# Kernel optimization log

Hardware: AMD Instinct MI355X
Metric: run time of the kernel (lower is better)

## Reference

```python
import jax, jax.numpy as jnp
import numpy as np

B, T, N, H = 1024, 256, 32, 64  # batch, SEQ_LEN, N_SERIES, RNN_HID_SIZE
EPS = 1e-05


def setup_inputs() -> dict:
    key = jax.random.key(0)
    ks = jax.random.split(key, 24)
    s_h = 1.0 / np.sqrt(H)
    s_n = 1.0 / np.sqrt(N)
    u = lambda k, shape, s: jax.random.uniform(k, shape, jnp.float32, -s, s)
    inp = {
        'values': jax.random.normal(ks[0], (B, T, N), jnp.float32),
        'masks': (jax.random.uniform(ks[1], (B, T, N)) < 0.8).astype(jnp.float32),
        'deltas': jax.random.uniform(ks[2], (B, T, N), jnp.float32) * 5.0,
        'evals': jax.random.normal(ks[3], (B, T, N), jnp.float32),
        'eval_masks': (jax.random.uniform(ks[4], (B, T, N)) < 0.1).astype(jnp.float32),
        'labels': (jax.random.uniform(ks[5], (B, 1)) < 0.5).astype(jnp.float32),
        'is_train': jnp.ones((B, 1), jnp.float32),
        # TemporalDecay h: Linear(N->H)
        'td_h_W': u(ks[6], (H, N), s_h), 'td_h_b': u(ks[7], (H,), s_h),
        # TemporalDecay x: diag Linear(N->N)
        'td_x_W': u(ks[8], (N, N), s_n), 'td_x_b': u(ks[9], (N,), s_n),
        # hist_reg: Linear(H->N)
        'hist_W': u(ks[10], (N, H), s_n), 'hist_b': u(ks[11], (N,), s_n),
        # feat_reg: masked Linear(N->N), mask = 1 - I
        'feat_W': u(ks[12], (N, N), s_n), 'feat_b': u(ks[13], (N,), s_n),
        # weight_combine: Linear(2N->N)
        'wc_W': u(ks[14], (N, 2 * N), s_n), 'wc_b': u(ks[15], (N,), s_n),
        # LSTMCell(2N -> H)
        'W_ih': u(ks[16], (4 * H, 2 * N), s_h), 'W_hh': u(ks[17], (4 * H, H), s_h),
        'b_ih': u(ks[18], (4 * H,), s_h), 'b_hh': u(ks[19], (4 * H,), s_h),
        # out: Linear(H->1)
        'out_W': u(ks[20], (1, H), s_h), 'out_b': u(ks[21], (1,), s_h),
    }
    return inp


def _rits_forward(values, masks, deltas, labels, is_train,
                  td_h_W, td_h_b, td_x_W, td_x_b, hist_W, hist_b,
                  feat_W, feat_b, wc_W, wc_b, W_ih, W_hh, b_ih, b_hh,
                  out_W, out_b):
    # time-major for scan: [T, B, N]
    vals_t = jnp.swapaxes(values, 0, 1)
    masks_t = jnp.swapaxes(masks, 0, 1)
    delts_t = jnp.swapaxes(deltas, 0, 1)

    feat_mask = 1.0 - jnp.eye(N, dtype=values.dtype)
    td_x_diag = jnp.diagonal(td_x_W)                  # W * eye(N) linear == elementwise diag

    def step(carry, xmd):
        h, c, x_loss = carry
        x, m, d = xmd
        gamma_h = jnp.exp(-jax.nn.relu(d @ td_h_W.T + td_h_b))   # [B,H]
        gamma_x = jnp.exp(-jax.nn.relu(d * td_x_diag + td_x_b))  # [B,N]
        h = h * gamma_h
        x_h = h @ hist_W.T + hist_b
        msum = jnp.sum(m) + EPS
        x_loss = x_loss + jnp.sum(jnp.abs(x - x_h) * m) / msum
        x_c = m * x + (1.0 - m) * x_h
        z_h = x_c @ (feat_W * feat_mask).T + feat_b
        x_loss = x_loss + jnp.sum(jnp.abs(x - z_h) * m) / msum
        alpha = jnp.concatenate([gamma_x, m], axis=1) @ wc_W.T + wc_b
        c_h = alpha * z_h + (1.0 - alpha) * x_h
        x_loss = x_loss + jnp.sum(jnp.abs(x - c_h) * m) / msum
        c_c = m * x + (1.0 - m) * c_h
        inputs = jnp.concatenate([c_c, m], axis=1)  # [B, 2N]
        gates = inputs @ W_ih.T + b_ih + h @ W_hh.T + b_hh
        i, f, g, o = jnp.split(gates, 4, axis=1)
        c = jax.nn.sigmoid(f) * c + jax.nn.sigmoid(i) * jnp.tanh(g)
        h = jax.nn.sigmoid(o) * jnp.tanh(c)
        return (h, c, x_loss), c_c

    h0 = jnp.zeros((values.shape[0], H), values.dtype)
    c0 = jnp.zeros((values.shape[0], H), values.dtype)
    (h, c, x_loss), imps = jax.lax.scan(step, (h0, c0, jnp.float32(0.0)),
                                        (vals_t, masks_t, delts_t))
    imputations = jnp.swapaxes(imps, 0, 1)  # [B, T, N]

    y_h = h @ out_W.T + out_b  # logits [B,1]
    # binary_cross_entropy_with_logits, reduce=False
    max_val = jnp.maximum(-y_h, 0.0)
    bce = y_h - y_h * labels + max_val + jnp.log(jnp.exp(-max_val) + jnp.exp(-y_h - max_val))
    y_loss = jnp.sum(bce * is_train) / (jnp.sum(is_train) + EPS)
    loss = x_loss / T + y_loss * 0.1
    predictions = jax.nn.sigmoid(y_h)
    return loss, predictions, imputations


def reference(values, masks, deltas, evals, eval_masks, labels, is_train,
              td_h_W, td_h_b, td_x_W, td_x_b, hist_W, hist_b, feat_W, feat_b,
              wc_W, wc_b, W_ih, W_hh, b_ih, b_hh, out_W, out_b):
    loss, predictions, imputations = _rits_forward(
        values, masks, deltas, labels, is_train,
        td_h_W, td_h_b, td_x_W, td_x_b, hist_W, hist_b,
        feat_W, feat_b, wc_W, wc_b, W_ih, W_hh, b_ih, b_hh, out_W, out_b)
    return loss, predictions, imputations
```

## Files before the change

### kernel.cpp

```cpp
#include <hip/hip_runtime.h>

#define EPSF 1e-5f

typedef _Float16 h2f  __attribute__((ext_vector_type(2)));
typedef _Float16 h8   __attribute__((ext_vector_type(8)));
typedef float    f32x4 __attribute__((ext_vector_type(4)));

#if defined(__has_builtin)
#if __has_builtin(__builtin_amdgcn_fdot2)
#define HAVE_FDOT2 1
#endif
#endif

__device__ __forceinline__ float fsig(float x){ return 1.0f/(1.0f+__expf(-x)); }
__device__ __forceinline__ float ftanh(float x){
  float e = __expf(2.f*x);
  float r = (e-1.f)/(e+1.f);
  return (x > 15.f) ? 1.f : ((x < -15.f) ? -1.f : r);
}
__device__ __forceinline__ int pkf(float lo, float hi){
  return __builtin_bit_cast(int, __builtin_amdgcn_cvt_pkrtz(lo, hi));
}
__device__ __forceinline__ int4 mk4(const float* p){
  return make_int4(pkf(p[0],p[1]),pkf(p[2],p[3]),pkf(p[4],p[5]),pkf(p[6],p[7]));
}
__device__ __forceinline__ float dot2(int w, int x, float acc){
#ifdef HAVE_FDOT2
  return __builtin_amdgcn_fdot2(__builtin_bit_cast(h2f, w),
                                __builtin_bit_cast(h2f, x), acc, false);
#else
  h2f a = __builtin_bit_cast(h2f, w), b = __builtin_bit_cast(h2f, x);
  return acc + (float)a[0]*(float)b[0] + (float)a[1]*(float)b[1];
#endif
}
__device__ __forceinline__ int rl_i(int v, int l){ return __builtin_amdgcn_readlane(v, l); }
__device__ __forceinline__ float rl_f(float v, int l){
  return __int_as_float(__builtin_amdgcn_readlane(__float_as_int(v), l));
}
#define MFMA(A,B,C) __builtin_amdgcn_mfma_f32_16x16x32_f16( \
    __builtin_bit_cast(h8,(A)), __builtin_bit_cast(h8,(B)), (C), 0,0,0)
#define BAR() do{ asm volatile("s_waitcnt lgkmcnt(0)" ::: "memory"); __builtin_amdgcn_s_barrier(); }while(0)

__global__ void msum_kernel(const float* __restrict__ masks, float* __restrict__ msum){
  const int t   = blockIdx.x;
  const int tid = threadIdx.x;
  const int b0  = tid >> 3;
  const int n4  = (tid & 7) << 2;
  float s = 0.f;
  #pragma unroll 4
  for (int i = 0; i < 32; ++i) {
    const int b = b0 + (i << 5);
    const float4 v = *reinterpret_cast<const float4*>(masks + ((size_t)b*256 + t)*32 + n4);
    s += v.x + v.y + v.z + v.w;
  }
  __shared__ float red[256];
  red[tid] = s; __syncthreads();
  for (int off = 128; off > 0; off >>= 1) {
    if (tid < off) red[tid] += red[tid + off];
    __syncthreads();
  }
  if (tid == 0) msum[t] = red[0] + EPSF;
}

__global__ __launch_bounds__(512)
__attribute__((amdgpu_waves_per_eu(2, 2)))
void rits_kernel(
  const float* __restrict__ values, const float* __restrict__ masks,
  const float* __restrict__ deltas, const float* __restrict__ labels,
  const float* __restrict__ is_train,
  const float* __restrict__ td_h_W, const float* __restrict__ td_h_b,
  const float* __restrict__ td_x_W, const float* __restrict__ td_x_b,
  const float* __restrict__ hist_W, const float* __restrict__ hist_b,
  const float* __restrict__ feat_W, const float* __restrict__ feat_b,
  const float* __restrict__ wc_W,  const float* __restrict__ wc_b,
  const float* __restrict__ W_ih,  const float* __restrict__ W_hh,
  const float* __restrict__ b_ih,  const float* __restrict__ b_hh,
  const float* __restrict__ out_W, const float* __restrict__ out_b,
  const float* __restrict__ msum,
  float* __restrict__ xl_acc, float* __restrict__ bce_acc,
  float* __restrict__ predictions, float* __restrict__ imps)
{
  __shared__ __align__(16) int  inp_s[4][84];
  __shared__ __align__(16) int  nb[4][52];
  __shared__ float sB[4][64];
  __shared__ float sAl[4][32];
  __shared__ float gp[4][256];
  __shared__ float msum_l[256];

  const int tid = threadIdx.x;
  const int b   = blockIdx.x;
  const int wv  = tid >> 6;
  const int ln  = tid & 63;
  const bool chain = (wv < 4);
  const int me  = wv & 3;
  const int b2  = (b << 2) | me;
  const int kg  = ln >> 4;
  const int arow = ln & 15;

  if (tid < 256) msum_l[tid] = 1.0f / msum[tid];

  int4 Wb[2][4];
  #pragma unroll
  for (int nt = 0; nt < 2; ++nt){
    const int col = (wv << 5) + (nt << 4) + (ln & 15);
    #pragma unroll
    for (int ks = 0; ks < 4; ++ks){
      const int k0 = (ks << 5) + (kg << 3);
      const float* src = (k0 < 64) ? (W_ih + (size_t)col*64 + k0)
                                   : (W_hh + (size_t)col*64 + (k0 - 64));
      Wb[nt][ks] = make_int4(pkf(src[0],src[1]), pkf(src[2],src[3]),
                             pkf(src[4],src[5]), pkf(src[6],src[7]));
    }
  }
  const int col0 = (wv << 5) + (ln & 15);
  const float bs0 = b_ih[col0]      + b_hh[col0];
  const float bs1 = b_ih[col0 + 16] + b_hh[col0 + 16];

  int4 fGh = make_int4(0,0,0,0);
  float ghb = 0.f; int colj = 0;
  int4 fA0 = make_int4(0,0,0,0), fA1 = make_int4(0,0,0,0);
  float alb = 0.f; int colA = 0;
  if (wv >= 4){
    colj = ((wv - 4) << 4) | (ln & 15);
    fGh  = mk4(td_h_W + colj*32 + kg*8);
    ghb  = td_h_b[colj];
    if (wv < 6){
      colA = ((wv - 4) << 4) | (ln & 15);
      fA0  = mk4(wc_W + colA*64 + kg*8);
      fA1  = mk4(wc_W + colA*64 + 32 + kg*8);
      alb  = wc_b[colA];
    }
  }

  int4  fC[8];
  float wz[32];
  float tdxd_r=0.f, tdxb_r=0.f, histb_r=0.f, featb_r=0.f;
  float xv=0.f, mv=0.f, dv=0.f;
  if (chain){
    const int nr = ln & 31;
    #pragma unroll
    for (int g = 0; g < 8; ++g) fC[g] = mk4(hist_W + nr*64 + 8*g);
    #pragma unroll
    for (int k = 0; k < 32; ++k) wz[k] = (k==nr) ? 0.f : feat_W[nr*32 + k];
    if (ln < 32){
      tdxd_r  = td_x_W[ln*33];
      tdxb_r  = td_x_b[ln];
      histb_r = hist_b[ln];
      featb_r = feat_b[ln];
      const size_t base = (size_t)b2*8192 + ln;
      xv = values[base]; mv = masks[base]; dv = deltas[base];
    }
  }
  float h_reg = 0.f, c_reg = 0.f, loss_acc = 0.f;
  const int i0 = (2*ln) & 63, i1 = (2*ln+1) & 63;

  __syncthreads();

  if (chain && ln < 32){
    _Float16* np = reinterpret_cast<_Float16*>(&nb[me][0]);
    const float gx0 = __expf(-fmaxf(fmaf(dv, tdxd_r, tdxb_r), 0.f));
    np[ln]      = (_Float16)dv;
    np[32 + ln] = (_Float16)gx0;
    np[64 + ln] = (_Float16)mv;
  }
  __syncthreads();
  if (wv >= 4){
    int4 A = make_int4(0,0,0,0);
    if (arow < 4) A = *reinterpret_cast<const int4*>(&nb[arow][kg << 2]);
    f32x4 acc = {ghb, ghb, ghb, ghb};
    acc = MFMA(A, fGh, acc);
    if (kg == 0){
      #pragma unroll
      for (int e = 0; e < 4; ++e) sB[e][colj] = acc[e];
    }
    if (wv < 6){
      int4 A0 = make_int4(0,0,0,0), A1 = make_int4(0,0,0,0);
      if (arow < 4){
        A0 = *reinterpret_cast<const int4*>(&nb[arow][16 + (kg << 2)]);
        A1 = *reinterpret_cast<const int4*>(&nb[arow][32 + (kg << 2)]);
      }
      f32x4 aacc = {alb, alb, alb, alb};
      aacc = MFMA(A0, fA0, aacc);
      aacc = MFMA(A1, fA1, aacc);
      if (kg == 0){
        #pragma unroll
        for (int e = 0; e < 4; ++e) sAl[e][colA] = aacc[e];
      }
    }
  }
  __syncthreads();

  for (int t = 0; t < 256; ++t){
    if (chain){
      const float x_cur = xv, m_cur = mv;
      const float sb = sB[me][ln];
      const float al = (ln < 32) ? sAl[me][ln] : 0.f;
      if (ln < 32 && t < 255){
        const size_t base = (size_t)b2*8192 + (size_t)(t+1)*32 + ln;
        xv = values[base]; mv = masks[base]; dv = deltas[base];
      }
      _Float16* hp = reinterpret_cast<_Float16*>(&inp_s[me][0]);
      _Float16* np = reinterpret_cast<_Float16*>(&nb[me][0]);

      h_reg *= __expf(-fmaxf(sb, 0.f));
      hp[64 + ln] = (_Float16)h_reg;
      const int hw = pkf(__shfl(h_reg, i0), __shfl(h_reg, i1));
      float xh_v = 0.f, x_c_v = 0.f;
      if (ln < 32){
        float a0 = histb_r, a1 = 0.f, a2 = 0.f, a3 = 0.f;
        #pragma unroll
        for (int g4 = 0; g4 < 8; ++g4){
          const int4 w = fC[g4];
          a0 = dot2(w.x, rl_i(hw, 4*g4+0), a0);
          a1 = dot2(w.y, rl_i(hw, 4*g4+1), a1);
          a2 = dot2(w.z, rl_i(hw, 4*g4+2), a2);
          a3 = dot2(w.w, rl_i(hw, 4*g4+3), a3);
        }
        xh_v  = (a0+a1)+(a2+a3);
        x_c_v = m_cur*x_cur + (1.f-m_cur)*xh_v;
      }
      if (ln < 32){
        float z0 = featb_r, z1 = 0.f, z2 = 0.f, z3 = 0.f;
        #pragma unroll
        for (int k = 0; k < 32; k += 4){
          z0 = fmaf(rl_f(x_c_v, k+0), wz[k+0], z0);
          z1 = fmaf(rl_f(x_c_v, k+1), wz[k+1], z1);
          z2 = fmaf(rl_f(x_c_v, k+2), wz[k+2], z2);
          z3 = fmaf(rl_f(x_c_v, k+3), wz[k+3], z3);
        }
        const float z = (z0+z1)+(z2+z3);
        const float ch = al*z + (1.f-al)*xh_v;
        loss_acc += (fabsf(x_cur-xh_v)+fabsf(x_cur-z)+fabsf(x_cur-ch))*m_cur*msum_l[t];
        const float ccv = m_cur*x_cur + (1.f-m_cur)*ch;
        imps[(size_t)b2*8192 + (size_t)t*32 + ln] = ccv;
        hp[ln]      = (_Float16)ccv;
        hp[32 + ln] = (_Float16)m_cur;
        const float gxn = __expf(-fmaxf(fmaf(dv, tdxd_r, tdxb_r), 0.f));
        np[ln]      = (_Float16)dv;
        np[32 + ln] = (_Float16)gxn;
        np[64 + ln] = (_Float16)mv;
      }
    }

    BAR();

    {
      int4 A[4];
      if (arow < 4){
        #pragma unroll
        for (int ks = 0; ks < 4; ++ks)
          A[ks] = *reinterpret_cast<const int4*>(&inp_s[arow][(ks << 4) + (kg << 2)]);
      } else {
        #pragma unroll
        for (int ks = 0; ks < 4; ++ks) A[ks] = make_int4(0,0,0,0);
      }
      f32x4 acc0 = {bs0, bs0, bs0, bs0};
      f32x4 acc1 = {bs1, bs1, bs1, bs1};
      #pragma unroll
      for (int ks = 0; ks < 4; ++ks){
        acc0 = __builtin_amdgcn_mfma_f32_16x16x32_f16(
                 __builtin_bit_cast(h8, A[ks]), __builtin_bit_cast(h8, Wb[0][ks]), acc0, 0,0,0);
        acc1 = __builtin_amdgcn_mfma_f32_16x16x32_f16(
                 __builtin_bit_cast(h8, A[ks]), __builtin_bit_cast(h8, Wb[1][ks]), acc1, 0,0,0);
      }
      if (kg == 0){
        #pragma unroll
        for (int e = 0; e < 4; ++e){
          gp[e][col0]      = acc0[e];
          gp[e][col0 + 16] = acc1[e];
        }
      }
    }
    if (wv >= 4){
      int4 Agh = make_int4(0,0,0,0);
      if (arow < 4) Agh = *reinterpret_cast<const int4*>(&nb[arow][kg << 2]);
      f32x4 accg = {ghb, ghb, ghb, ghb};
      accg = MFMA(Agh, fGh, accg);
      if (kg == 0){
        #pragma unroll
        for (int e = 0; e < 4; ++e) sB[e][colj] = accg[e];
      }
      if (wv < 6){
        int4 A0 = make_int4(0,0,0,0), A1 = make_int4(0,0,0,0);
        if (arow < 4){
          A0 = *reinterpret_cast<const int4*>(&nb[arow][16 + (kg << 2)]);
          A1 = *reinterpret_cast<const int4*>(&nb[arow][32 + (kg << 2)]);
        }
        f32x4 aacc = {alb, alb, alb, alb};
        aacc = MFMA(A0, fA0, aacc);
        aacc = MFMA(A1, fA1, aacc);
        if (kg == 0){
          #pragma unroll
          for (int e = 0; e < 4; ++e) sAl[e][colA] = aacc[e];
        }
      }
    }

    BAR();

    if (chain){
      const float ig = gp[me][ln];
      const float fg = gp[me][64+ln];
      const float gg = gp[me][128+ln];
      const float og = gp[me][192+ln];
      c_reg = fsig(fg)*c_reg + fsig(ig)*ftanh(gg);
      h_reg = fsig(og)*ftanh(c_reg);
    }
  }

  if (chain){
    float l = loss_acc;
    l += __shfl_xor(l,16); l += __shfl_xor(l,8);
    l += __shfl_xor(l,4);  l += __shfl_xor(l,2); l += __shfl_xor(l,1);
    if (ln == 0) atomicAdd(xl_acc, l);

    float p = h_reg * out_W[ln];
    p += __shfl_xor(p,32); p += __shfl_xor(p,16); p += __shfl_xor(p,8);
    p += __shfl_xor(p,4);  p += __shfl_xor(p,2);  p += __shfl_xor(p,1);
    if (ln == 0){
      const float y = p + out_b[0];
      predictions[b2] = fsig(y);
      const float lab = labels[b2];
      const float it  = is_train[b2];
      const float mx  = fmaxf(-y, 0.f);
      const float bce = y - y*lab + mx + __logf(__expf(-mx) + __expf(-y - mx));
      atomicAdd(bce_acc, bce * it);
    }
  }
}

__global__ void final_kernel(const float* __restrict__ is_train,
                             const float* __restrict__ ws,
                             float* __restrict__ out){
  const int tid = threadIdx.x;
  __shared__ float red[256];
  red[tid] = is_train[tid] + is_train[tid+256] + is_train[tid+512] + is_train[tid+768];
  __syncthreads();
  for (int off = 128; off > 0; off >>= 1){
    if (tid < off) red[tid] += red[tid + off];
    __syncthreads();
  }
  if (tid == 0){
    const float yl = ws[1] / (red[0] + EPSF);
    out[0] = ws[0] / 256.0f + 0.1f * yl;
  }
}

extern "C" void kernel_launch(void* const* d_in, const int* in_sizes, int n_in,
                              void* d_out, int out_size, void* d_ws, size_t ws_size,
                              hipStream_t stream){
  const float* values   = (const float*)d_in[0];
  const float* masks    = (const float*)d_in[1];
  const float* deltas   = (const float*)d_in[2];
  const float* labels   = (const float*)d_in[5];
  const float* is_train = (const float*)d_in[6];
  const float* td_h_W   = (const float*)d_in[7];
  const float* td_h_b   = (const float*)d_in[8];
  const float* td_x_W   = (const float*)d_in[9];
  const float* td_x_b   = (const float*)d_in[10];
  const float* hist_W   = (const float*)d_in[11];
  const float* hist_b   = (const float*)d_in[12];
  const float* feat_W   = (const float*)d_in[13];
  const float* feat_b   = (const float*)d_in[14];
  const float* wc_W     = (const float*)d_in[15];
  const float* wc_b     = (const float*)d_in[16];
  const float* W_ih     = (const float*)d_in[17];
  const float* W_hh     = (const float*)d_in[18];
  const float* b_ih     = (const float*)d_in[19];
  const float* b_hh     = (const float*)d_in[20];
  const float* out_W    = (const float*)d_in[21];
  const float* out_b    = (const float*)d_in[22];

  float* out = (float*)d_out;
  float* ws  = (float*)d_ws;

  hipMemsetAsync(ws, 0, 2*sizeof(float), stream);
  msum_kernel<<<256, 256, 0, stream>>>(masks, ws + 2);
  rits_kernel<<<256, 512, 0, stream>>>(values, masks, deltas, labels, is_train,
      td_h_W, td_h_b, td_x_W, td_x_b, hist_W, hist_b, feat_W, feat_b,
      wc_W, wc_b, W_ih, W_hh, b_ih, b_hh, out_W, out_b,
      ws + 2, ws + 0, ws + 1, out + 1, out + 1 + 1024);
  final_kernel<<<1, 256, 0, stream>>>(is_train, ws, out);
}
```

Measured before the change: 379.2 us.

## Pack eight batch rows per block and split chain and MFMA waves

Each block now handles eight batch rows (128 blocks of 1024 threads) instead of four, using 8 of the 16 MFMA rows. Waves 0-7 now only do the elementwise chain work, and waves 8-15 do all the gate, decay and weight-combine MFMAs. The goal is to double useful rows per MFMA and halve the block count so all blocks fit in one wave on the device. The cost is a larger per-block barrier and a serial handoff between chain waves and MFMA waves, with no overlap between them.

```diff
diff --git a/kernel.cpp b/kernel.cpp
--- a/kernel.cpp
+++ b/kernel.cpp
@@ -62,8 +62,7 @@
   if (tid == 0) msum[t] = red[0] + EPSF;
 }
 
-__global__ __launch_bounds__(512)
-__attribute__((amdgpu_waves_per_eu(2, 2)))
+__global__ __launch_bounds__(1024, 1)
 void rits_kernel(
   const float* __restrict__ values, const float* __restrict__ masks,
   const float* __restrict__ deltas, const float* __restrict__ labels,
@@ -80,52 +79,55 @@
   float* __restrict__ xl_acc, float* __restrict__ bce_acc,
   float* __restrict__ predictions, float* __restrict__ imps)
 {
-  __shared__ __align__(16) int  inp_s[4][84];
-  __shared__ __align__(16) int  nb[4][52];
-  __shared__ float sB[4][64];
-  __shared__ float sAl[4][32];
-  __shared__ float gp[4][256];
+  __shared__ __align__(16) int  inp_s[8][84];
+  __shared__ __align__(16) int  nb[8][52];
+  __shared__ float sB[8][64];
+  __shared__ float sAl[8][32];
+  __shared__ float gp[8][256];
   __shared__ float msum_l[256];
 
   const int tid = threadIdx.x;
   const int b   = blockIdx.x;
   const int wv  = tid >> 6;
   const int ln  = tid & 63;
-  const bool chain = (wv < 4);
-  const int me  = wv & 3;
-  const int b2  = (b << 2) | me;
+  const bool chain = (wv < 8);
+  const int me  = wv & 7;
+  const int ew  = wv - 8;
+  const int b2  = (b << 3) | me;
   const int kg  = ln >> 4;
   const int arow = ln & 15;
 
   if (tid < 256) msum_l[tid] = 1.0f / msum[tid];
 
   int4 Wb[2][4];
-  #pragma unroll
-  for (int nt = 0; nt < 2; ++nt){
-    const int col = (wv << 5) + (nt << 4) + (ln & 15);
-    #pragma unroll
-    for (int ks = 0; ks < 4; ++ks){
-      const int k0 = (ks << 5) + (kg << 3);
-      const float* src = (k0 < 64) ? (W_ih + (size_t)col*64 + k0)
-                                   : (W_hh + (size_t)col*64 + (k0 - 64));
-      Wb[nt][ks] = make_int4(pkf(src[0],src[1]), pkf(src[2],src[3]),
-                             pkf(src[4],src[5]), pkf(src[6],src[7]));
-    }
-  }
-  const int col0 = (wv << 5) + (ln & 15);
-  const float bs0 = b_ih[col0]      + b_hh[col0];
-  const float bs1 = b_ih[col0 + 16] + b_hh[col0 + 16];
-
+  float bs0 = 0.f, bs1 = 0.f; int col0 = 0;
   int4 fGh = make_int4(0,0,0,0);
   float ghb = 0.f; int colj = 0;
   int4 fA0 = make_int4(0,0,0,0), fA1 = make_int4(0,0,0,0);
   float alb = 0.f; int colA = 0;
-  if (wv >= 4){
-    colj = ((wv - 4) << 4) | (ln & 15);
-    fGh  = mk4(td_h_W + colj*32 + kg*8);
-    ghb  = td_h_b[colj];
-    if (wv < 6){
-      colA = ((wv - 4) << 4) | (ln & 15);
+  if (!chain){
+    #pragma unroll
+    for (int nt = 0; nt < 2; ++nt){
+      const int col = (ew << 5) + (nt << 4) + (ln & 15);
+      #pragma unroll
+      for (int ks = 0; ks < 4; ++ks){
+        const int k0 = (ks << 5) + (kg << 3);
+        const float* src = (k0 < 64) ? (W_ih + (size_t)col*64 + k0)
+                                     : (W_hh + (size_t)col*64 + (k0 - 64));
+        Wb[nt][ks] = make_int4(pkf(src[0],src[1]), pkf(src[2],src[3]),
+                               pkf(src[4],src[5]), pkf(src[6],src[7]));
+      }
+    }
+    col0 = (ew << 5) + (ln & 15);
+    bs0 = b_ih[col0]      + b_hh[col0];
+    bs1 = b_ih[col0 + 16] + b_hh[col0 + 16];
+    if (ew < 4){
+      colj = (ew << 4) | (ln & 15);
+      fGh  = mk4(td_h_W + colj*32 + kg*8);
+      ghb  = td_h_b[colj];
+    }
+    if (ew == 4 || ew == 5){
+      colA = ((ew - 4) << 4) | (ln & 15);
       fA0  = mk4(wc_W + colA*64 + kg*8);
       fA1  = mk4(wc_W + colA*64 + 32 + kg*8);
       alb  = wc_b[colA];
@@ -164,27 +166,29 @@
     np[64 + ln] = (_Float16)mv;
   }
   __syncthreads();
-  if (wv >= 4){
-    int4 A = make_int4(0,0,0,0);
-    if (arow < 4) A = *reinterpret_cast<const int4*>(&nb[arow][kg << 2]);
-    f32x4 acc = {ghb, ghb, ghb, ghb};
-    acc = MFMA(A, fGh, acc);
-    if (kg == 0){
-      #pragma unroll
-      for (int e = 0; e < 4; ++e) sB[e][colj] = acc[e];
-    }
-    if (wv < 6){
+  if (!chain){
+    if (ew < 4){
+      int4 A = make_int4(0,0,0,0);
+      if (arow < 8) A = *reinterpret_cast<const int4*>(&nb[arow][kg << 2]);
+      f32x4 acc = {ghb, ghb, ghb, ghb};
+      acc = MFMA(A, fGh, acc);
+      if (kg < 2){
+        #pragma unroll
+        for (int e = 0; e < 4; ++e) sB[(kg<<2)+e][colj] = acc[e];
+      }
+    }
+    if (ew == 4 || ew == 5){
       int4 A0 = make_int4(0,0,0,0), A1 = make_int4(0,0,0,0);
-      if (arow < 4){
+      if (arow < 8){
         A0 = *reinterpret_cast<const int4*>(&nb[arow][16 + (kg << 2)]);
         A1 = *reinterpret_cast<const int4*>(&nb[arow][32 + (kg << 2)]);
       }
       f32x4 aacc = {alb, alb, alb, alb};
       aacc = MFMA(A0, fA0, aacc);
       aacc = MFMA(A1, fA1, aacc);
-      if (kg == 0){
-        #pragma unroll
-        for (int e = 0; e < 4; ++e) sAl[e][colA] = aacc[e];
+      if (kg < 2){
+        #pragma unroll
+        for (int e = 0; e < 4; ++e) sAl[(kg<<2)+e][colA] = aacc[e];
       }
     }
   }
@@ -244,9 +248,9 @@
 
     BAR();
 
-    {
+    if (!chain){
       int4 A[4];
-      if (arow < 4){
+      if (arow < 8){
         #pragma unroll
         for (int ks = 0; ks < 4; ++ks)
           A[ks] = *reinterpret_cast<const int4*>(&inp_s[arow][(ks << 4) + (kg << 2)]);
@@ -263,35 +267,35 @@
         acc1 = __builtin_amdgcn_mfma_f32_16x16x32_f16(
                  __builtin_bit_cast(h8, A[ks]), __builtin_bit_cast(h8, Wb[1][ks]), acc1, 0,0,0);
       }
-      if (kg == 0){
+      if (kg < 2){
         #pragma unroll
         for (int e = 0; e < 4; ++e){
-          gp[e][col0]      = acc0[e];
-          gp[e][col0 + 16] = acc1[e];
-        }
-      }
-    }
-    if (wv >= 4){
-      int4 Agh = make_int4(0,0,0,0);
-      if (arow < 4) Agh = *reinterpret_cast<const int4*>(&nb[arow][kg << 2]);
-      f32x4 accg = {ghb, ghb, ghb, ghb};
-      accg = MFMA(Agh, fGh, accg);
-      if (kg == 0){
-        #pragma unroll
-        for (int e = 0; e < 4; ++e) sB[e][colj] = accg[e];
-      }
-      if (wv < 6){
+          gp[(kg<<2)+e][col0]      = acc0[e];
+          gp[(kg<<2)+e][col0 + 16] = acc1[e];
+        }
+      }
+      if (ew < 4){
+        int4 Agh = make_int4(0,0,0,0);
+        if (arow < 8) Agh = *reinterpret_cast<const int4*>(&nb[arow][kg << 2]);
+        f32x4 accg = {ghb, ghb, ghb, ghb};
+        accg = MFMA(Agh, fGh, accg);
+        if (kg < 2){
+          #pragma unroll
+          for (int e = 0; e < 4; ++e) sB[(kg<<2)+e][colj] = accg[e];
+        }
+      }
+      if (ew == 4 || ew == 5){
         int4 A0 = make_int4(0,0,0,0), A1 = make_int4(0,0,0,0);
-        if (arow < 4){
+        if (arow < 8){
           A0 = *reinterpret_cast<const int4*>(&nb[arow][16 + (kg << 2)]);
           A1 = *reinterpret_cast<const int4*>(&nb[arow][32 + (kg << 2)]);
         }
         f32x4 aacc = {alb, alb, alb, alb};
         aacc = MFMA(A0, fA0, aacc);
         aacc = MFMA(A1, fA1, aacc);
-        if (kg == 0){
+        if (kg < 2){
           #pragma unroll
-          for (int e = 0; e < 4; ++e) sAl[e][colA] = aacc[e];
+          for (int e = 0; e < 4; ++e) sAl[(kg<<2)+e][colA] = aacc[e];
         }
       }
     }
@@ -376,7 +380,7 @@
 
   hipMemsetAsync(ws, 0, 2*sizeof(float), stream);
   msum_kernel<<<256, 256, 0, stream>>>(masks, ws + 2);
-  rits_kernel<<<256, 512, 0, stream>>>(values, masks, deltas, labels, is_train,
+  rits_kernel<<<128, 1024, 0, stream>>>(values, masks, deltas, labels, is_train,
       td_h_W, td_h_b, td_x_W, td_x_b, hist_W, hist_b, feat_W, feat_b,
       wc_W, wc_b, W_ih, W_hh, b_ih, b_hh, out_W, out_b,
       ws + 2, ws + 0, ws + 1, out + 1, out + 1 + 1024);
```

Result: slower. 1.238 ms (+226.6%).
